# Kernel tuning notes

Measured on AMD Instinct MI355X. Metric: run time of the kernel, lower is better.

Reference implementation:

```python
import jax, jax.numpy as jnp
import numpy as np

NN_SIZE = 16  # nn_size from __init__


def _knn_idx(points_ref, k):
    """Brute-force KNN of points_ref against itself (replaces faiss_knn).
    Returns (B, N, k) neighbor indices, self point excluded."""
    sq = jnp.sum(points_ref * points_ref, axis=-1)  # (B, N)
    # squared pairwise distances (B, N, N)
    d2 = sq[:, :, None] + sq[:, None, :] - 2.0 * jnp.einsum(
        'bnd,bmd->bnm', points_ref, points_ref)
    _, idx = jax.lax.top_k(-d2, k + 1)  # nearest first; idx[...,0] is self
    return idx[:, :, 1:]


def _edge_lengths(pts, knn_idx):
    """Gather neighbor coords and compute edge lengths (B, N, K)."""
    group = jax.vmap(lambda p, i: p[i])(pts, knn_idx)  # (B, N, K, D)
    return jnp.linalg.norm(group - pts[:, :, None, :], axis=-1)


def setup_inputs() -> dict:
    key = jax.random.key(0)
    k1, k2 = jax.random.split(key)
    B, N, D = 4, 8192, 3
    points_ref = jax.random.normal(k1, (B, N, D), dtype=jnp.float32)
    # pred points: perturbed ref so the loss is non-degenerate
    points = points_ref + 0.01 * jax.random.normal(k2, (B, N, D), dtype=jnp.float32)
    return {"points_ref": points_ref, "points": points}


def reference(points_ref, points):
    # faiss KNN is non-differentiable -> stop_gradient on the index search
    knn_idx = _knn_idx(jax.lax.stop_gradient(points_ref), NN_SIZE)  # (B,N,K)
    dist_ref = _edge_lengths(points_ref, knn_idx)  # (B, N, K)
    dist = _edge_lengths(points, knn_idx)          # (B, N, K)
    # metric = torch.nn.L1Loss() (mean reduction)
    return jnp.mean(jnp.abs(dist_ref - dist))
```

## Files before the change

kernel.cpp:

```cpp
#include <hip/hip_runtime.h>
#include <math.h>

#define BATCH 4
#define NPTS  8192
#define KNN   16
#define KK    17
#define NQ    (BATCH*NPTS)
#define JMASK 0x1FFFu
#define EMASK 0xFFFFE000u
#define TOTAL_EDGES (BATCH*NPTS*KNN)

#define GC    32
#define GLO   (-4.5f)
#define GINV  (32.0f/9.0f)
#define NCELL (GC*GC*GC)

#define NSG   512
#define SGS   16

#define QPW   8
#define GRIDQ (NQ/QPW)
#define WIN   64

__device__ __forceinline__ int cell_coord(float x) {
    int c = (int)floorf((x - GLO) * GINV);
    return min(GC - 1, max(0, c));
}
__device__ __forceinline__ unsigned spread5(unsigned v) {
    v &= 31u;
    v = (v | (v << 8)) & 0x100Fu;
    v = (v | (v << 4)) & 0x10C3u;
    v = (v | (v << 2)) & 0x1249u;
    return v;
}
__device__ __forceinline__ unsigned morton_id(float x, float y, float z) {
    return spread5((unsigned)cell_coord(x)) | (spread5((unsigned)cell_coord(y)) << 1)
         | (spread5((unsigned)cell_coord(z)) << 2);
}
__device__ __forceinline__ unsigned mkkey(const float4 p, float xi, float yi,
                                          float zi, float sqi, unsigned j) {
    const float e  = fmaf(p.x, xi, fmaf(p.y, yi, p.z * zi)) + p.w;
    const float d2 = e + sqi;
    return (__float_as_uint(d2) & EMASK) | j;
}
__device__ __forceinline__ void ins17(unsigned (&a)[KK], unsigned key) {
    #pragma unroll
    for (int k = KK - 1; k >= 1; --k) a[k] = min(a[k], max(a[k - 1], key));
    a[0] = min(a[0], key);
}

__global__ void pel_hist(const float* __restrict__ pref, unsigned* __restrict__ hist,
                         float* __restrict__ acc, unsigned* __restrict__ bcnt) {
    const int idx = blockIdx.x * 256 + threadIdx.x;
    if (idx == 0) { acc[0] = 0.0f; bcnt[0] = 0u; }
    const int b = idx >> 13;
    const unsigned mid = morton_id(pref[3*idx], pref[3*idx+1], pref[3*idx+2]);
    atomicAdd(&hist[b * NCELL + mid], 1u);
}
__global__ __launch_bounds__(1024)
void pel_scan(const unsigned* __restrict__ hist, unsigned* __restrict__ off) {
    __shared__ unsigned s[1024];
    const unsigned* h = hist + blockIdx.x * NCELL;
    unsigned*       o = off  + blockIdx.x * NCELL;
    const int t = threadIdx.x;
    unsigned v[32], tot = 0;
    #pragma unroll
    for (int k = 0; k < 32; ++k) { v[k] = h[t * 32 + k]; tot += v[k]; }
    s[t] = tot;
    __syncthreads();
    for (int d = 1; d < 1024; d <<= 1) {
        const unsigned add = (t >= d) ? s[t - d] : 0u;
        __syncthreads();
        s[t] += add;
        __syncthreads();
    }
    unsigned run = s[t] - tot;
    #pragma unroll
    for (int k = 0; k < 32; ++k) { o[t * 32 + k] = run; run += v[k]; }
}
__global__ void pel_scatter(const float* __restrict__ pref, const float* __restrict__ pts,
                            unsigned* __restrict__ off,
                            float4* __restrict__ p4r, float4* __restrict__ p4p) {
    const int idx = blockIdx.x * 256 + threadIdx.x;
    const int b = idx >> 13;
    const float x = pref[3*idx], y = pref[3*idx+1], z = pref[3*idx+2];
    const unsigned mid = morton_id(x, y, z);
    const unsigned pos = atomicAdd(&off[b * NCELL + mid], 1u);
    p4r[b * NPTS + pos] = make_float4(-2.f*x, -2.f*y, -2.f*z, fmaf(x, x, fmaf(y, y, z*z)));
    const float px = pts[3*idx], py = pts[3*idx+1], pz = pts[3*idx+2];
    p4p[b * NPTS + pos] = make_float4(-2.f*px, -2.f*py, -2.f*pz,
                                      fmaf(px, px, fmaf(py, py, pz*pz)));
}
__global__ __launch_bounds__(256)
void pel_gstat(const float4* __restrict__ P4r, float4* __restrict__ sgball) {
    const int quad = threadIdx.x >> 4, pos = threadIdx.x & 15;
    const int gid = blockIdx.x * 16 + quad;
    const int b = gid >> 9, s = gid & (NSG - 1);
    const float4 p = P4r[b * NPTS + s * SGS + pos];
    const float x = -0.5f * p.x, y = -0.5f * p.y, z = -0.5f * p.z;
    float mnx = x, mxx = x, mny = y, mxy = y, mnz = z, mxz = z;
    #pragma unroll
    for (int m = 1; m <= 8; m <<= 1) {
        mnx = fminf(mnx, __shfl_xor(mnx, m, 64)); mxx = fmaxf(mxx, __shfl_xor(mxx, m, 64));
        mny = fminf(mny, __shfl_xor(mny, m, 64)); mxy = fmaxf(mxy, __shfl_xor(mxy, m, 64));
        mnz = fminf(mnz, __shfl_xor(mnz, m, 64)); mxz = fmaxf(mxz, __shfl_xor(mxz, m, 64));
    }
    const float cx = 0.5f * (mnx + mxx), cy = 0.5f * (mny + mxy), cz = 0.5f * (mnz + mxz);
    float d = sqrtf((x-cx)*(x-cx) + (y-cy)*(y-cy) + (z-cz)*(z-cz));
    #pragma unroll
    for (int m = 1; m <= 8; m <<= 1) d = fmaxf(d, __shfl_xor(d, m, 64));
    if (pos == 0) sgball[gid] = make_float4(cx, cy, cz, d);
}

__global__ __launch_bounds__(64, 4)
void pel_query(const float4* __restrict__ P4r, const float4* __restrict__ P4p,
               const float4* __restrict__ sgball,
               float* __restrict__ acc_ws, unsigned* __restrict__ bcnt,
               float* __restrict__ out)
{
    __shared__ unsigned short s_list[NSG];

    const int lane = threadIdx.x;
    const int lq = lane >> 3, sp = lane & 7;
    const int q  = blockIdx.x * QPW + lq;
    const int b  = q >> 13;
    const int i  = q & (NPTS - 1);

    const float4* __restrict__ Pq = P4r + b * NPTS;
    const float4* __restrict__ Pp = P4p + b * NPTS;
    const float4* __restrict__ Sg = sgball + b * NSG;

    const float4 self = Pq[i];
    const float xi = -0.5f * self.x, yi = -0.5f * self.y, zi = -0.5f * self.z;
    const float sqi = self.w;

    unsigned a3[3] = {~0u, ~0u, ~0u};
    const int wln = min(max(i - WIN / 2, 0), NPTS - WIN) + sp * 8;
    #pragma unroll
    for (int u = 0; u < 8; ++u) {
        const unsigned key = mkkey(Pq[wln + u], xi, yi, zi, sqi, (unsigned)(wln + u));
        a3[2] = min(a3[2], max(a3[1], key));
        a3[1] = min(a3[1], max(a3[0], key));
        a3[0] = min(a3[0], key);
    }
    unsigned tb;
    {
        const unsigned v0  = a3[2];
        const unsigned v1  = (unsigned)__shfl_xor((int)v0, 1, 64);
        const unsigned A   = max(v0, v1), B = min(v0, v1);
        const unsigned A2  = (unsigned)__shfl_xor((int)A, 2, 64);
        const unsigned B2  = (unsigned)__shfl_xor((int)B, 2, 64);
        const unsigned S   = max(A, A2);
        const unsigned U   = max(min(A, A2), max(B, B2));
        const unsigned S4  = (unsigned)__shfl_xor((int)S, 4, 64);
        const unsigned U4  = (unsigned)__shfl_xor((int)U, 4, 64);
        tb = max(min(S, S4), max(U, U4));
    }
    const unsigned bound = tb;
    const float rt = sqrtf(__uint_as_float((bound & EMASK) + 0x2000u));

    float mnx = xi, mxx = xi, mny = yi, mxy = yi, mnz = zi, mxz = zi;
    #pragma unroll
    for (int m = 1; m <= 32; m <<= 1) {
        mnx = fminf(mnx, __shfl_xor(mnx, m, 64)); mxx = fmaxf(mxx, __shfl_xor(mxx, m, 64));
        mny = fminf(mny, __shfl_xor(mny, m, 64)); mxy = fmaxf(mxy, __shfl_xor(mxy, m, 64));
        mnz = fminf(mnz, __shfl_xor(mnz, m, 64)); mxz = fmaxf(mxz, __shfl_xor(mxz, m, 64));
    }
    const float cxw = 0.5f * (mnx + mxx), cyw = 0.5f * (mny + mxy), czw = 0.5f * (mnz + mxz);
    float v = sqrtf((xi-cxw)*(xi-cxw) + (yi-cyw)*(yi-cyw) + (zi-czw)*(zi-czw)) + rt;
    #pragma unroll
    for (int m = 1; m <= 32; m <<= 1) v = fmaxf(v, __shfl_xor(v, m, 64));
    const float Rq = v + 1e-3f;

    int ng = 0;
    #pragma unroll
    for (int r = 0; r < NSG / 64; ++r) {
        const int k2 = r * 64 + lane;
        const float4 gb = Sg[k2];
        const float dx = gb.x - cxw, dy = gb.y - cyw, dz = gb.z - czw;
        const float rhs = Rq + gb.w;
        const bool acc = (dx*dx + dy*dy + dz*dz <= rhs * rhs);
        const unsigned long long mask = __ballot(acc);
        if (acc)
            s_list[ng + (int)__popcll(mask & ((1ull << lane) - 1ull))] = (unsigned short)k2;
        ng += (int)__popcll(mask);
    }
    __syncthreads();

    unsigned c17[KK];
    #pragma unroll
    for (int k = 0; k < KK; ++k) c17[k] = 0xFFFFFFFFu;
    unsigned tauL = bound;
    const int sp2 = sp * 2;
    int j0 = (int)s_list[0] * SGS + sp2;
    int j1 = (int)s_list[min(1, ng - 1)] * SGS + sp2;
    float4 c0a = Pq[j0], c0b = Pq[j0 + 1];
    float4 c1a = Pq[j1], c1b = Pq[j1 + 1];
    for (int e = 0; e < ng; ++e) {
        const int jn = (int)s_list[min(e + 2, ng - 1)] * SGS + sp2;
        const float4 nxa = Pq[jn], nxb = Pq[jn + 1];
        unsigned key = mkkey(c0a, xi, yi, zi, sqi, (unsigned)j0);
        if (key <= tauL) { ins17(c17, key); tauL = min(tauL, c17[KK - 1]); }
        key = mkkey(c0b, xi, yi, zi, sqi, (unsigned)(j0 + 1));
        if (key <= tauL) { ins17(c17, key); tauL = min(tauL, c17[KK - 1]); }
        c0a = c1a; c0b = c1b; j0 = j1;
        c1a = nxa; c1b = nxb; j1 = jn;
    }

    unsigned cpy[KK];
    #pragma unroll
    for (int k = 0; k < KK; ++k) cpy[k] = c17[k];
    unsigned tauK = 0xFFFFFFFFu;
    for (int r = 0; r < KK; ++r) {
        const unsigned h  = cpy[0];
        unsigned m1 = min(h,  (unsigned)__shfl_xor((int)h,  1, 64));
        m1          = min(m1, (unsigned)__shfl_xor((int)m1, 2, 64));
        const unsigned w = min(m1, (unsigned)__shfl_xor((int)m1, 4, 64));
        const bool won = (h == w);
        #pragma unroll
        for (int k = 0; k < KK - 1; ++k) cpy[k] = won ? cpy[k + 1] : cpy[k];
        cpy[KK - 1] = won ? 0xFFFFFFFFu : cpy[KK - 1];
        tauK = w;
    }

    const float4 selfp = Pp[i];
    const float pxi = -0.5f * selfp.x, pyi = -0.5f * selfp.y, pzi = -0.5f * selfp.z;
    float accv = 0.0f;
    #pragma unroll
    for (int k = 0; k < KK; ++k) {
        if (c17[k] <= tauK) {
            const int j = (int)(c17[k] & JMASK);
            const float4 pr = Pq[j];
            const float er  = fmaf(pr.x, xi, fmaf(pr.y, yi, pr.z * zi)) + pr.w;
            const float d2r = fmaxf(er + sqi, 0.0f);
            const float4 pp = Pp[j];
            const float ep  = fmaf(pp.x, pxi, fmaf(pp.y, pyi, pp.z * pzi)) + pp.w;
            const float d2p = fmaxf(ep + selfp.w, 0.0f);
            accv += fabsf(sqrtf(d2r) - sqrtf(d2p));
        }
    }

    #pragma unroll
    for (int o = 32; o > 0; o >>= 1) accv += __shfl_down(accv, o, 64);
    if (lane == 0) {
        atomicAdd(acc_ws, accv);
        __threadfence();
        const unsigned old = atomicAdd(bcnt, 1u);
        if (old == GRIDQ - 1) {
            __threadfence();
            const float total = atomicAdd(acc_ws, 0.0f);
            out[0] = total * (1.0f / (float)TOTAL_EDGES);
        }
    }
}

extern "C" void kernel_launch(void* const* d_in, const int* in_sizes, int n_in,
                              void* d_out, int out_size, void* d_ws, size_t ws_size,
                              hipStream_t stream) {
    const float* pref = (const float*)d_in[0];
    const float* pts  = (const float*)d_in[1];
    float4*   P4r  = (float4*)d_ws;
    float4*   P4p  = P4r + NQ;
    unsigned* hist = (unsigned*)d_ws;
    unsigned* off  = (unsigned*)((char*)d_ws + 1048576);
    float4*   sgball = (float4*)((char*)d_ws + 1048576);
    float*    acc  = (float*)((char*)d_ws + 1581056);
    unsigned* bcnt = (unsigned*)(acc + 1);
    float*    out  = (float*)d_out;

    hipMemsetAsync(hist, 0, BATCH * NCELL * sizeof(unsigned), stream);
    pel_hist   <<<NQ / 256, 256, 0, stream>>>(pref, hist, acc, bcnt);
    pel_scan   <<<BATCH, 1024, 0, stream>>>(hist, off);
    pel_scatter<<<NQ / 256, 256, 0, stream>>>(pref, pts, off, P4r, P4p);
    pel_gstat  <<<(BATCH * NSG) / 16, 256, 0, stream>>>(P4r, sgball);
    pel_query  <<<GRIDQ, 64, 0, stream>>>(P4r, P4p, sgball, acc, bcnt, out);
}
```

Baseline: 309.5 us.

## Replace subgroup-ball culling with per-wave brute-force slice scan and LDS merge

Removes the subgroup bounding-ball kernel and the spatial pruning. Each block now handles 64 queries with 8 waves, and each wave scans a full 1024-point slice with a threshold seeded from a local window. The per-wave top-17 lists are merged through shared memory, and the edge-loss evaluation is split across waves. This removes the cull and divergence overhead but scans every point for every query, and the dynamic indexing of the register array may spill.

```diff
diff --git a/kernel.cpp b/kernel.cpp
--- a/kernel.cpp
+++ b/kernel.cpp
@@ -15,11 +15,11 @@
 #define GINV  (32.0f/9.0f)
 #define NCELL (GC*GC*GC)
 
-#define NSG   512
-#define SGS   16
-
-#define QPW   8
-#define GRIDQ (NQ/QPW)
+#define QPB   64
+#define BLOCK 512
+#define NWAVE 8
+#define SLICE (NPTS/NWAVE)
+#define GRIDQ (NQ/QPB)
 #define WIN   64
 
 __device__ __forceinline__ int cell_coord(float x) {
@@ -91,159 +91,96 @@
     p4p[b * NPTS + pos] = make_float4(-2.f*px, -2.f*py, -2.f*pz,
                                       fmaf(px, px, fmaf(py, py, pz*pz)));
 }
-__global__ __launch_bounds__(256)
-void pel_gstat(const float4* __restrict__ P4r, float4* __restrict__ sgball) {
-    const int quad = threadIdx.x >> 4, pos = threadIdx.x & 15;
-    const int gid = blockIdx.x * 16 + quad;
-    const int b = gid >> 9, s = gid & (NSG - 1);
-    const float4 p = P4r[b * NPTS + s * SGS + pos];
-    const float x = -0.5f * p.x, y = -0.5f * p.y, z = -0.5f * p.z;
-    float mnx = x, mxx = x, mny = y, mxy = y, mnz = z, mxz = z;
-    #pragma unroll
-    for (int m = 1; m <= 8; m <<= 1) {
-        mnx = fminf(mnx, __shfl_xor(mnx, m, 64)); mxx = fmaxf(mxx, __shfl_xor(mxx, m, 64));
-        mny = fminf(mny, __shfl_xor(mny, m, 64)); mxy = fmaxf(mxy, __shfl_xor(mxy, m, 64));
-        mnz = fminf(mnz, __shfl_xor(mnz, m, 64)); mxz = fmaxf(mxz, __shfl_xor(mxz, m, 64));
-    }
-    const float cx = 0.5f * (mnx + mxx), cy = 0.5f * (mny + mxy), cz = 0.5f * (mnz + mxz);
-    float d = sqrtf((x-cx)*(x-cx) + (y-cy)*(y-cy) + (z-cz)*(z-cz));
-    #pragma unroll
-    for (int m = 1; m <= 8; m <<= 1) d = fmaxf(d, __shfl_xor(d, m, 64));
-    if (pos == 0) sgball[gid] = make_float4(cx, cy, cz, d);
-}
-
-__global__ __launch_bounds__(64, 4)
+
+__global__ __launch_bounds__(BLOCK, 4)
 void pel_query(const float4* __restrict__ P4r, const float4* __restrict__ P4p,
-               const float4* __restrict__ sgball,
                float* __restrict__ acc_ws, unsigned* __restrict__ bcnt,
                float* __restrict__ out)
 {
-    __shared__ unsigned short s_list[NSG];
-
-    const int lane = threadIdx.x;
-    const int lq = lane >> 3, sp = lane & 7;
-    const int q  = blockIdx.x * QPW + lq;
-    const int b  = q >> 13;
-    const int i  = q & (NPTS - 1);
+    __shared__ unsigned s_pool[KK][BLOCK];
+    __shared__ float s_part[NWAVE];
+
+    const int t = threadIdx.x;
+    const int l = t & 63, w = t >> 6;
+    const int q = blockIdx.x * QPB + l;
+    const int b = q >> 13;
+    const int i = q & (NPTS - 1);
 
     const float4* __restrict__ Pq = P4r + b * NPTS;
     const float4* __restrict__ Pp = P4p + b * NPTS;
-    const float4* __restrict__ Sg = sgball + b * NSG;
 
     const float4 self = Pq[i];
     const float xi = -0.5f * self.x, yi = -0.5f * self.y, zi = -0.5f * self.z;
     const float sqi = self.w;
 
-    unsigned a3[3] = {~0u, ~0u, ~0u};
-    const int wln = min(max(i - WIN / 2, 0), NPTS - WIN) + sp * 8;
-    #pragma unroll
-    for (int u = 0; u < 8; ++u) {
-        const unsigned key = mkkey(Pq[wln + u], xi, yi, zi, sqi, (unsigned)(wln + u));
-        a3[2] = min(a3[2], max(a3[1], key));
-        a3[1] = min(a3[1], max(a3[0], key));
-        a3[0] = min(a3[0], key);
-    }
-    unsigned tb;
-    {
-        const unsigned v0  = a3[2];
-        const unsigned v1  = (unsigned)__shfl_xor((int)v0, 1, 64);
-        const unsigned A   = max(v0, v1), B = min(v0, v1);
-        const unsigned A2  = (unsigned)__shfl_xor((int)A, 2, 64);
-        const unsigned B2  = (unsigned)__shfl_xor((int)B, 2, 64);
-        const unsigned S   = max(A, A2);
-        const unsigned U   = max(min(A, A2), max(B, B2));
-        const unsigned S4  = (unsigned)__shfl_xor((int)S, 4, 64);
-        const unsigned U4  = (unsigned)__shfl_xor((int)U, 4, 64);
-        tb = max(min(S, S4), max(U, U4));
-    }
-    const unsigned bound = tb;
-    const float rt = sqrtf(__uint_as_float((bound & EMASK) + 0x2000u));
-
-    float mnx = xi, mxx = xi, mny = yi, mxy = yi, mnz = zi, mxz = zi;
-    #pragma unroll
-    for (int m = 1; m <= 32; m <<= 1) {
-        mnx = fminf(mnx, __shfl_xor(mnx, m, 64)); mxx = fmaxf(mxx, __shfl_xor(mxx, m, 64));
-        mny = fminf(mny, __shfl_xor(mny, m, 64)); mxy = fmaxf(mxy, __shfl_xor(mxy, m, 64));
-        mnz = fminf(mnz, __shfl_xor(mnz, m, 64)); mxz = fmaxf(mxz, __shfl_xor(mxz, m, 64));
-    }
-    const float cxw = 0.5f * (mnx + mxx), cyw = 0.5f * (mny + mxy), czw = 0.5f * (mnz + mxz);
-    float v = sqrtf((xi-cxw)*(xi-cxw) + (yi-cyw)*(yi-cyw) + (zi-czw)*(zi-czw)) + rt;
-    #pragma unroll
-    for (int m = 1; m <= 32; m <<= 1) v = fmaxf(v, __shfl_xor(v, m, 64));
-    const float Rq = v + 1e-3f;
-
-    int ng = 0;
-    #pragma unroll
-    for (int r = 0; r < NSG / 64; ++r) {
-        const int k2 = r * 64 + lane;
-        const float4 gb = Sg[k2];
-        const float dx = gb.x - cxw, dy = gb.y - cyw, dz = gb.z - czw;
-        const float rhs = Rq + gb.w;
-        const bool acc = (dx*dx + dy*dy + dz*dz <= rhs * rhs);
-        const unsigned long long mask = __ballot(acc);
-        if (acc)
-            s_list[ng + (int)__popcll(mask & ((1ull << lane) - 1ull))] = (unsigned short)k2;
-        ng += (int)__popcll(mask);
-    }
+    unsigned t17[KK];
+    #pragma unroll
+    for (int k = 0; k < KK; ++k) t17[k] = 0xFFFFFFFFu;
+    const int w0 = min(max(i - WIN / 2, 0), NPTS - WIN);
+    for (int u = 0; u < WIN; ++u) {
+        const unsigned key = mkkey(Pq[w0 + u], xi, yi, zi, sqi, (unsigned)(w0 + u));
+        if (key <= t17[KK - 1]) ins17(t17, key);
+    }
+    unsigned tauL = t17[KK - 1];
+
+    unsigned c17[KK];
+    #pragma unroll
+    for (int k = 0; k < KK; ++k) c17[k] = 0xFFFFFFFFu;
+    const int jb = w << 10;
+    float4 p0 = Pq[jb], p1 = Pq[jb + 1], p2 = Pq[jb + 2], p3 = Pq[jb + 3];
+    for (int j = 0; j < SLICE; j += 4) {
+        const int jn = jb + ((j + 4) & (SLICE - 1));
+        const float4 n0 = Pq[jn],     n1 = Pq[jn + 1];
+        const float4 n2 = Pq[jn + 2], n3 = Pq[jn + 3];
+        unsigned key;
+        key = mkkey(p0, xi, yi, zi, sqi, (unsigned)(jb + j));
+        if (key <= tauL) { ins17(c17, key); tauL = min(tauL, c17[KK - 1]); }
+        key = mkkey(p1, xi, yi, zi, sqi, (unsigned)(jb + j + 1));
+        if (key <= tauL) { ins17(c17, key); tauL = min(tauL, c17[KK - 1]); }
+        key = mkkey(p2, xi, yi, zi, sqi, (unsigned)(jb + j + 2));
+        if (key <= tauL) { ins17(c17, key); tauL = min(tauL, c17[KK - 1]); }
+        key = mkkey(p3, xi, yi, zi, sqi, (unsigned)(jb + j + 3));
+        if (key <= tauL) { ins17(c17, key); tauL = min(tauL, c17[KK - 1]); }
+        p0 = n0; p1 = n1; p2 = n2; p3 = n3;
+    }
+
+    #pragma unroll
+    for (int k = 0; k < KK; ++k) s_pool[k][t] = c17[k];
     __syncthreads();
-
-    unsigned c17[KK];
-    #pragma unroll
-    for (int k = 0; k < KK; ++k) c17[k] = 0xFFFFFFFFu;
-    unsigned tauL = bound;
-    const int sp2 = sp * 2;
-    int j0 = (int)s_list[0] * SGS + sp2;
-    int j1 = (int)s_list[min(1, ng - 1)] * SGS + sp2;
-    float4 c0a = Pq[j0], c0b = Pq[j0 + 1];
-    float4 c1a = Pq[j1], c1b = Pq[j1 + 1];
-    for (int e = 0; e < ng; ++e) {
-        const int jn = (int)s_list[min(e + 2, ng - 1)] * SGS + sp2;
-        const float4 nxa = Pq[jn], nxb = Pq[jn + 1];
-        unsigned key = mkkey(c0a, xi, yi, zi, sqi, (unsigned)j0);
-        if (key <= tauL) { ins17(c17, key); tauL = min(tauL, c17[KK - 1]); }
-        key = mkkey(c0b, xi, yi, zi, sqi, (unsigned)(j0 + 1));
-        if (key <= tauL) { ins17(c17, key); tauL = min(tauL, c17[KK - 1]); }
-        c0a = c1a; c0b = c1b; j0 = j1;
-        c1a = nxa; c1b = nxb; j1 = jn;
-    }
-
-    unsigned cpy[KK];
-    #pragma unroll
-    for (int k = 0; k < KK; ++k) cpy[k] = c17[k];
-    unsigned tauK = 0xFFFFFFFFu;
-    for (int r = 0; r < KK; ++r) {
-        const unsigned h  = cpy[0];
-        unsigned m1 = min(h,  (unsigned)__shfl_xor((int)h,  1, 64));
-        m1          = min(m1, (unsigned)__shfl_xor((int)m1, 2, 64));
-        const unsigned w = min(m1, (unsigned)__shfl_xor((int)m1, 4, 64));
-        const bool won = (h == w);
-        #pragma unroll
-        for (int k = 0; k < KK - 1; ++k) cpy[k] = won ? cpy[k + 1] : cpy[k];
-        cpy[KK - 1] = won ? 0xFFFFFFFFu : cpy[KK - 1];
-        tauK = w;
+    #pragma unroll 1
+    for (int d = 1; d < NWAVE; ++d) {
+        const int t2 = (((w + d) & (NWAVE - 1)) << 6) | l;
+        #pragma unroll 1
+        for (int k = 0; k < KK; ++k) {
+            const unsigned vk = s_pool[k][t2];
+            if (vk >= c17[KK - 1]) break;
+            ins17(c17, vk);
+        }
     }
 
     const float4 selfp = Pp[i];
     const float pxi = -0.5f * selfp.x, pyi = -0.5f * selfp.y, pzi = -0.5f * selfp.z;
     float accv = 0.0f;
-    #pragma unroll
-    for (int k = 0; k < KK; ++k) {
-        if (c17[k] <= tauK) {
-            const int j = (int)(c17[k] & JMASK);
-            const float4 pr = Pq[j];
-            const float er  = fmaf(pr.x, xi, fmaf(pr.y, yi, pr.z * zi)) + pr.w;
-            const float d2r = fmaxf(er + sqi, 0.0f);
-            const float4 pp = Pp[j];
-            const float ep  = fmaf(pp.x, pxi, fmaf(pp.y, pyi, pp.z * pzi)) + pp.w;
-            const float d2p = fmaxf(ep + selfp.w, 0.0f);
-            accv += fabsf(sqrtf(d2r) - sqrtf(d2p));
-        }
+    for (int r = w; r < KK; r += NWAVE) {
+        const int j = (int)(c17[r] & JMASK);
+        const float4 pr = Pq[j];
+        const float er  = fmaf(pr.x, xi, fmaf(pr.y, yi, pr.z * zi)) + pr.w;
+        const float d2r = fmaxf(er + sqi, 0.0f);
+        const float4 pp = Pp[j];
+        const float ep  = fmaf(pp.x, pxi, fmaf(pp.y, pyi, pp.z * pzi)) + pp.w;
+        const float d2p = fmaxf(ep + selfp.w, 0.0f);
+        accv += fabsf(sqrtf(d2r) - sqrtf(d2p));
     }
 
     #pragma unroll
     for (int o = 32; o > 0; o >>= 1) accv += __shfl_down(accv, o, 64);
-    if (lane == 0) {
-        atomicAdd(acc_ws, accv);
+    if (l == 0) s_part[w] = accv;
+    __syncthreads();
+    if (t == 0) {
+        float s = 0.0f;
+        #pragma unroll
+        for (int w2 = 0; w2 < NWAVE; ++w2) s += s_part[w2];
+        atomicAdd(acc_ws, s);
         __threadfence();
         const unsigned old = atomicAdd(bcnt, 1u);
         if (old == GRIDQ - 1) {
@@ -263,7 +200,6 @@
     float4*   P4p  = P4r + NQ;
     unsigned* hist = (unsigned*)d_ws;
     unsigned* off  = (unsigned*)((char*)d_ws + 1048576);
-    float4*   sgball = (float4*)((char*)d_ws + 1048576);
     float*    acc  = (float*)((char*)d_ws + 1581056);
     unsigned* bcnt = (unsigned*)(acc + 1);
     float*    out  = (float*)d_out;
@@ -272,6 +208,5 @@
     pel_hist   <<<NQ / 256, 256, 0, stream>>>(pref, hist, acc, bcnt);
     pel_scan   <<<BATCH, 1024, 0, stream>>>(hist, off);
     pel_scatter<<<NQ / 256, 256, 0, stream>>>(pref, pts, off, P4r, P4p);
-    pel_gstat  <<<(BATCH * NSG) / 16, 256, 0, stream>>>(P4r, sgball);
-    pel_query  <<<GRIDQ, 64, 0, stream>>>(P4r, P4p, sgball, acc, bcnt, out);
-}
+    pel_query  <<<GRIDQ, BLOCK, 0, stream>>>(P4r, P4p, acc, bcnt, out);
+}
```

Result: faster. 261.9 us (-15.4%).
